# Performance work log

Measured on AMD Instinct MI355X. Metric: run time of the kernel, lower is better.

The kernel has to match this reference:

```python
import jax, jax.numpy as jnp
import numpy as np

B, S, H, OUT = 64, 513, 1024, 128   # batch, seq (incl CLS), hidden, slot labels
T = S - 1                            # subword tokens after dropping [CLS]
P_WORD_START = 0.75                  # avg ~1.33 subwords per word


def setup_inputs() -> dict:
    key = jax.random.key(0)
    k1, k2, k3, k4 = jax.random.split(key, 4)
    hidden_states = jax.random.normal(k1, (B, S, H), jnp.float32)
    W = jax.random.normal(k2, (H, OUT), jnp.float32) * 0.02
    b = jax.random.normal(k3, (OUT,), jnp.float32) * 0.02
    # contiguous, non-decreasing word ids: cumsum of word-start flags
    starts = (jax.random.uniform(k4, (B, T)) < P_WORD_START).astype(jnp.int32)
    starts = starts.at[:, 0].set(1)
    segment_ids = jnp.cumsum(starts, axis=-1) - 1  # [B, T], values in [0, n_words)
    return {"hidden_states": hidden_states, "W": W, "b": b,
            "segment_ids": segment_ids}


def _merge_row(logits, seg):
    # logits: [T, OUT], seg: [T] contiguous non-decreasing word ids
    s = jax.ops.segment_sum(logits, seg, num_segments=T)                    # [T, OUT]
    c = jax.ops.segment_sum(jnp.ones((T,), logits.dtype), seg, num_segments=T)
    mean = s / jnp.maximum(c, 1.0)[:, None]
    # words beyond n_words (empty segments) -> zero padding, as in the original
    return jnp.where(c[:, None] > 0, mean, 0.0)


def reference(hidden_states, W, b, segment_ids):
    x = hidden_states[:, 1:]                       # drop [CLS]; dropout = identity (eval)
    logits = jnp.einsum('bth,ho->bto', x, W) + b   # [B, T, OUT]
    merged = jax.vmap(_merge_row)(logits, segment_ids)  # per-word ragged mean + pad
    return jnp.transpose(merged, (0, 2, 1))        # [B, OUT, T]
```

## Files before the change

kernel.cpp:

```cpp
#include <hip/hip_runtime.h>
#include <hip/hip_bf16.h>

#define B_    64
#define S_    513
#define T_    512
#define H_    1024
#define OUT_  128
#define BK    32
#define BN    32
#define NKT   (H_ / BK)

typedef __attribute__((ext_vector_type(8))) short short8_t;
typedef __attribute__((ext_vector_type(4))) float f32x4;

__device__ inline ushort f2bf(float f) {
    union { float f; unsigned u; } x; x.f = f;
    unsigned r = x.u + 0x7fffu + ((x.u >> 16) & 1u);
    return (ushort)(r >> 16);
}

union SmemT {
    struct {
        ushort As[2][T_ * BK];
        ushort Bs[2][BN * BK];
    } st;
    float lg[T_ * 33];
};

__global__ __launch_bounds__(512, 2) void fused_kernel(
    const float* __restrict__ hs, const float* __restrict__ W,
    const float* __restrict__ bias, const int* __restrict__ seg,
    float* __restrict__ out)
{
    __shared__ SmemT sm;
    __shared__ int s_start[T_];
    __shared__ int s_cnt[T_];

    int d = blockIdx.x;
    int batch = (d & 7) + ((d >> 5) << 3);
    int o0    = ((d >> 3) & 3) * BN;

    int tid  = threadIdx.x;
    int lane = tid & 63;
    int w    = tid >> 6;
    int l15  = lane & 15, ksl = lane >> 4;

    s_start[tid] = T_;
    s_cnt[tid]   = 0;
    __syncthreads();
    {
        int sid = seg[batch * T_ + tid];
        atomicMin(&s_start[sid], tid);
        atomicAdd(&s_cnt[sid], 1);
    }

    int arow = tid >> 3;
    int ac8  = tid & 7;
    const float* aptr = hs + ((size_t)(batch * S_ + 1 + arow)) * H_ + ac8 * 4;
    int wAbase = arow * BK + ((((ac8 >> 1) ^ ((arow >> 1) & 3))) << 3)
               + ((ac8 & 1) << 2);

    int wk = tid >> 4;
    int wo = (tid & 15) * 2;
    const float* wptr = W + (size_t)wk * OUT_ + o0 + wo;
    int wBo0 = wo * BK + (((wk >> 3) ^ ((wo >> 1) & 3)) << 3) + (wk & 7);

    int rAo[4], rBo[2];
#pragma unroll
    for (int fm = 0; fm < 4; ++fm) {
        int row = w * 64 + fm * 16 + l15;
        rAo[fm] = row * BK + ((ksl ^ ((row >> 1) & 3)) << 3);
    }
#pragma unroll
    for (int fn = 0; fn < 2; ++fn) {
        int o = fn * 16 + l15;
        rBo[fn] = o * BK + ((ksl ^ ((o >> 1) & 3)) << 3);
    }

    f32x4 acc[4][2];
#pragma unroll
    for (int fm = 0; fm < 4; ++fm)
#pragma unroll
        for (int fn = 0; fn < 2; ++fn) acc[fm][fn] = (f32x4){0.f, 0.f, 0.f, 0.f};

    float4 ra[8];
    float2 rw;

    auto loadT = [&](int kt) {
        const float* ap = aptr + kt * BK;
#pragma unroll
        for (int p = 0; p < 8; ++p)
            ra[p] = *reinterpret_cast<const float4*>(ap + (size_t)p * 64 * H_);
        rw = *reinterpret_cast<const float2*>(wptr + (size_t)kt * BK * OUT_);
    };
    auto writeT = [&](int nb) {
#pragma unroll
        for (int p = 0; p < 8; ++p) {
            union { ushort u[4]; uint2 v; } pk;
            pk.u[0] = f2bf(ra[p].x); pk.u[1] = f2bf(ra[p].y);
            pk.u[2] = f2bf(ra[p].z); pk.u[3] = f2bf(ra[p].w);
            *reinterpret_cast<uint2*>(&sm.st.As[nb][wAbase + p * 64 * BK]) = pk.v;
        }
        sm.st.Bs[nb][wBo0]      = f2bf(rw.x);
        sm.st.Bs[nb][wBo0 + BK] = f2bf(rw.y);
    };
    auto computeT = [&](int cb) {
        short8_t af[4], bfr[2];
#pragma unroll
        for (int fm = 0; fm < 4; ++fm)
            af[fm] = *reinterpret_cast<const short8_t*>(&sm.st.As[cb][rAo[fm]]);
#pragma unroll
        for (int fn = 0; fn < 2; ++fn)
            bfr[fn] = *reinterpret_cast<const short8_t*>(&sm.st.Bs[cb][rBo[fn]]);
#pragma unroll
        for (int fm = 0; fm < 4; ++fm)
#pragma unroll
            for (int fn = 0; fn < 2; ++fn)
                acc[fm][fn] = __builtin_amdgcn_mfma_f32_16x16x32_bf16(
                    af[fm], bfr[fn], acc[fm][fn], 0, 0, 0);
    };

    loadT(0);
    writeT(0);
    __syncthreads();

    for (int kt = 0; kt < NKT; ++kt) {
        int cb = kt & 1;
        if (kt + 1 < NKT) loadT(kt + 1);
        computeT(cb);
        if (kt + 1 < NKT) writeT(cb ^ 1);
        __syncthreads();
    }

    float bv0 = bias[o0 + l15];
    float bv1 = bias[o0 + 16 + l15];
#pragma unroll
    for (int fm = 0; fm < 4; ++fm) {
#pragma unroll
        for (int fn = 0; fn < 2; ++fn) {
            float bv = fn ? bv1 : bv0;
            int o = fn * 16 + l15;
#pragma unroll
            for (int r = 0; r < 4; ++r) {
                int t = w * 64 + fm * 16 + ksl * 4 + r;
                sm.lg[t * 33 + o] = acc[fm][fn][r] + bv;
            }
        }
    }
    __syncthreads();

#pragma unroll
    for (int it = 0; it < 32; ++it) {
        int idx = tid + it * 512;
        int o   = idx >> 9;
        int s   = idx & 511;
        int cnt = s_cnt[s];
        float v = 0.f;
        if (cnt > 0) {
            int st = s_start[s];
            float sum = 0.f;
            for (int i = 0; i < cnt; ++i)
                sum += sm.lg[(st + i) * 33 + o];
            v = sum / (float)cnt;
        }
        out[((size_t)batch * OUT_ + o0 + o) * T_ + s] = v;
    }
}

extern "C" void kernel_launch(void* const* d_in, const int* in_sizes, int n_in,
                              void* d_out, int out_size, void* d_ws, size_t ws_size,
                              hipStream_t stream) {
    const float* hs   = (const float*)d_in[0];
    const float* W    = (const float*)d_in[1];
    const float* bias = (const float*)d_in[2];
    const int*   seg  = (const int*)d_in[3];
    float* out = (float*)d_out;

    fused_kernel<<<B_ * (OUT_ / BN), 512, 0, stream>>>(hs, W, bias, seg, out);
}
```

Baseline: 59.42 us.

## Tile over tokens instead of outputs, pretranspose W to bf16, and handle halo segments

The fused kernel used to have each block handle a full 512-token row for 32 output columns, so every hidden-state row was read four times. Now each block owns 64 tokens across all 128 outputs and loads up to 96 rows so that words crossing the tile edge can be finished locally. A separate small kernel first converts W to bf16 and transposes it into the workspace, so B fragments can be loaded straight into registers without going through LDS. The costs are an extra kernel launch, halo rows that are loaded and multiplied redundantly, and more involved boundary logic for segments that span tiles. Bias is now added after the mean, and tile 7 zero-fills the output for empty trailing words.

```diff
diff --git a/kernel.cpp b/kernel.cpp
--- a/kernel.cpp
+++ b/kernel.cpp
@@ -7,8 +7,10 @@
 #define H_    1024
 #define OUT_  128
 #define BK    32
-#define BN    32
 #define NKT   (H_ / BK)
+#define ROWS  96
+#define OWN   64
+#define LGS   132
 
 typedef __attribute__((ext_vector_type(8))) short short8_t;
 typedef __attribute__((ext_vector_type(4))) float f32x4;
@@ -18,152 +20,188 @@
     unsigned r = x.u + 0x7fffu + ((x.u >> 16) & 1u);
     return (ushort)(r >> 16);
 }
-
-union SmemT {
-    struct {
-        ushort As[2][T_ * BK];
-        ushort Bs[2][BN * BK];
-    } st;
-    float lg[T_ * 33];
-};
-
-__global__ __launch_bounds__(512, 2) void fused_kernel(
-    const float* __restrict__ hs, const float* __restrict__ W,
+__device__ inline int4 pack8(const float4& a, const float4& b) {
+    union { ushort u[8]; int4 v; } pk;
+    pk.u[0] = f2bf(a.x); pk.u[1] = f2bf(a.y); pk.u[2] = f2bf(a.z); pk.u[3] = f2bf(a.w);
+    pk.u[4] = f2bf(b.x); pk.u[5] = f2bf(b.y); pk.u[6] = f2bf(b.z); pk.u[7] = f2bf(b.w);
+    return pk.v;
+}
+
+__global__ __launch_bounds__(256) void wt_kernel(
+    const float* __restrict__ W, ushort* __restrict__ Wt)
+{
+    __shared__ ushort tile[64][65];
+    int k0 = blockIdx.x * 64, o0 = blockIdx.y * 64;
+    int tid = threadIdx.x;
+#pragma unroll
+    for (int p = 0; p < 16; ++p) {
+        int idx = tid + p * 256;
+        int r = idx >> 6, c = idx & 63;
+        tile[r][c] = f2bf(W[(size_t)(k0 + r) * OUT_ + o0 + c]);
+    }
+    __syncthreads();
+#pragma unroll
+    for (int p = 0; p < 16; ++p) {
+        int idx = tid + p * 256;
+        int c = idx >> 6, r = idx & 63;
+        Wt[(size_t)(o0 + c) * H_ + k0 + r] = tile[r][c];
+    }
+}
+
+__global__ __launch_bounds__(256, 2) void fused_kernel(
+    const float* __restrict__ hs, const ushort* __restrict__ Wt,
     const float* __restrict__ bias, const int* __restrict__ seg,
     float* __restrict__ out)
 {
-    __shared__ SmemT sm;
-    __shared__ int s_start[T_];
-    __shared__ int s_cnt[T_];
-
-    int d = blockIdx.x;
-    int batch = (d & 7) + ((d >> 5) << 3);
-    int o0    = ((d >> 3) & 3) * BN;
+    union Smem {
+        ushort As[2][ROWS * BK];
+        float  lg[ROWS * LGS];
+    };
+    __shared__ Smem sm;
+    __shared__ int sseg[ROWS];
+    __shared__ int lstart[OWN];
+    __shared__ int lcnt[OWN];
+    __shared__ int sExt, sSlo;
+
+    int bid  = blockIdx.x;
+    int b    = bid >> 3;
+    int tile = bid & 7;
+    int t0   = tile * OWN;
+    int Tl   = (T_ - t0) < ROWS ? (T_ - t0) : ROWS;
 
     int tid  = threadIdx.x;
     int lane = tid & 63;
     int w    = tid >> 6;
+    int wm   = w & 1, wn = w >> 1;
     int l15  = lane & 15, ksl = lane >> 4;
 
-    s_start[tid] = T_;
-    s_cnt[tid]   = 0;
-    __syncthreads();
-    {
-        int sid = seg[batch * T_ + tid];
-        atomicMin(&s_start[sid], tid);
-        atomicAdd(&s_cnt[sid], 1);
-    }
-
-    int arow = tid >> 3;
-    int ac8  = tid & 7;
-    const float* aptr = hs + ((size_t)(batch * S_ + 1 + arow)) * H_ + ac8 * 4;
-    int wAbase = arow * BK + ((((ac8 >> 1) ^ ((arow >> 1) & 3))) << 3)
-               + ((ac8 & 1) << 2);
-
-    int wk = tid >> 4;
-    int wo = (tid & 15) * 2;
-    const float* wptr = W + (size_t)wk * OUT_ + o0 + wo;
-    int wBo0 = wo * BK + (((wk >> 3) ^ ((wo >> 1) & 3)) << 3) + (wk & 7);
-
-    int rAo[4], rBo[2];
-#pragma unroll
-    for (int fm = 0; fm < 4; ++fm) {
-        int row = w * 64 + fm * 16 + l15;
-        rAo[fm] = row * BK + ((ksl ^ ((row >> 1) & 3)) << 3);
-    }
-#pragma unroll
-    for (int fn = 0; fn < 2; ++fn) {
-        int o = fn * 16 + l15;
-        rBo[fn] = o * BK + ((ksl ^ ((o >> 1) & 3)) << 3);
-    }
-
-    f32x4 acc[4][2];
-#pragma unroll
-    for (int fm = 0; fm < 4; ++fm)
-#pragma unroll
-        for (int fn = 0; fn < 2; ++fn) acc[fm][fn] = (f32x4){0.f, 0.f, 0.f, 0.f};
-
-    float4 ra[8];
-    float2 rw;
-
-    auto loadT = [&](int kt) {
-        const float* ap = aptr + kt * BK;
-#pragma unroll
-        for (int p = 0; p < 8; ++p)
-            ra[p] = *reinterpret_cast<const float4*>(ap + (size_t)p * 64 * H_);
-        rw = *reinterpret_cast<const float2*>(wptr + (size_t)kt * BK * OUT_);
-    };
-    auto writeT = [&](int nb) {
-#pragma unroll
-        for (int p = 0; p < 8; ++p) {
-            union { ushort u[4]; uint2 v; } pk;
-            pk.u[0] = f2bf(ra[p].x); pk.u[1] = f2bf(ra[p].y);
-            pk.u[2] = f2bf(ra[p].z); pk.u[3] = f2bf(ra[p].w);
-            *reinterpret_cast<uint2*>(&sm.st.As[nb][wAbase + p * 64 * BK]) = pk.v;
+    if (tid < Tl)  sseg[tid] = seg[b * T_ + t0 + tid];
+    if (tid < OWN) { lstart[tid] = ROWS; lcnt[tid] = 0; }
+    if (tid == 0)  sExt = Tl;
+    __syncthreads();
+    if (tid == 0) {
+        int start0 = (t0 == 0) || (seg[b * T_ + t0 - 1] != sseg[0]);
+        sSlo = sseg[0] + (start0 ? 0 : 1);
+    }
+    if (tid >= OWN && tid < Tl && sseg[tid] != sseg[tid - 1])
+        atomicMin(&sExt, tid);
+    __syncthreads();
+    int ext  = sExt;
+    int s_lo = sSlo;
+    int s_hi = sseg[OWN - 1] + 1;
+    if (tid < ext && sseg[tid] >= s_lo) {
+        int li = sseg[tid] - s_lo;
+        atomicMin(&lstart[li], tid);
+        atomicAdd(&lcnt[li], 1);
+    }
+
+    int arow0 = tid >> 2;
+    int ac    = tid & 3;
+    int arow1 = 64 + arow0;
+    const float* aptr0 = hs + ((size_t)(b * S_ + 1 + t0 + arow0)) * H_ + ac * 8;
+    const float* aptr1 = hs + ((size_t)(b * S_ + 1 + t0 + arow1)) * H_ + ac * 8;
+    bool doC1 = (tid < 128) && (arow1 < ext);
+    int wA0 = arow0 * BK + ac * 8;
+    int wA1 = arow1 * BK + ac * 8;
+
+    const ushort* bp[4];
+#pragma unroll
+    for (int fn = 0; fn < 4; ++fn)
+        bp[fn] = Wt + (size_t)(wn * 64 + fn * 16 + l15) * H_ + ksl * 8;
+
+    f32x4 acc[3][4];
+#pragma unroll
+    for (int fm = 0; fm < 3; ++fm)
+#pragma unroll
+        for (int fn = 0; fn < 4; ++fn) acc[fm][fn] = (f32x4){0.f, 0.f, 0.f, 0.f};
+
+    float4 ra0, ra1, ra2, ra3;
+    short8_t bfA[4], bfB[4];
+
+    auto loadA = [&](int kt) {
+        const float* p = aptr0 + kt * BK;
+        ra0 = *reinterpret_cast<const float4*>(p);
+        ra1 = *reinterpret_cast<const float4*>(p + 4);
+        if (doC1) {
+            const float* q = aptr1 + kt * BK;
+            ra2 = *reinterpret_cast<const float4*>(q);
+            ra3 = *reinterpret_cast<const float4*>(q + 4);
         }
-        sm.st.Bs[nb][wBo0]      = f2bf(rw.x);
-        sm.st.Bs[nb][wBo0 + BK] = f2bf(rw.y);
-    };
-    auto computeT = [&](int cb) {
-        short8_t af[4], bfr[2];
-#pragma unroll
-        for (int fm = 0; fm < 4; ++fm)
-            af[fm] = *reinterpret_cast<const short8_t*>(&sm.st.As[cb][rAo[fm]]);
-#pragma unroll
-        for (int fn = 0; fn < 2; ++fn)
-            bfr[fn] = *reinterpret_cast<const short8_t*>(&sm.st.Bs[cb][rBo[fn]]);
-#pragma unroll
-        for (int fm = 0; fm < 4; ++fm)
-#pragma unroll
-            for (int fn = 0; fn < 2; ++fn)
+    };
+    auto loadB = [&](short8_t* dst, int kt) {
+#pragma unroll
+        for (int fn = 0; fn < 4; ++fn)
+            dst[fn] = *reinterpret_cast<const short8_t*>(bp[fn] + kt * BK);
+    };
+    auto writeA = [&](int nb) {
+        *reinterpret_cast<int4*>(&sm.As[nb][wA0]) = pack8(ra0, ra1);
+        if (doC1)
+            *reinterpret_cast<int4*>(&sm.As[nb][wA1]) = pack8(ra2, ra3);
+    };
+    auto compute = [&](int cb, short8_t* bf) {
+        short8_t af[3];
+#pragma unroll
+        for (int fm = 0; fm < 3; ++fm)
+            af[fm] = *reinterpret_cast<const short8_t*>(
+                &sm.As[cb][(wm * 48 + fm * 16 + l15) * BK + ksl * 8]);
+#pragma unroll
+        for (int fm = 0; fm < 3; ++fm)
+#pragma unroll
+            for (int fn = 0; fn < 4; ++fn)
                 acc[fm][fn] = __builtin_amdgcn_mfma_f32_16x16x32_bf16(
-                    af[fm], bfr[fn], acc[fm][fn], 0, 0, 0);
-    };
-
-    loadT(0);
-    writeT(0);
-    __syncthreads();
-
-    for (int kt = 0; kt < NKT; ++kt) {
-        int cb = kt & 1;
-        if (kt + 1 < NKT) loadT(kt + 1);
-        computeT(cb);
-        if (kt + 1 < NKT) writeT(cb ^ 1);
+                    af[fm], bf[fn], acc[fm][fn], 0, 0, 0);
+    };
+
+    loadB(bfA, 0); loadA(0);
+    writeA(0);
+    __syncthreads();
+
+    for (int kt = 0; kt < NKT; kt += 2) {
+        loadA(kt + 1); loadB(bfB, kt + 1);
+        compute(0, bfA);
+        writeA(1);
         __syncthreads();
-    }
-
-    float bv0 = bias[o0 + l15];
-    float bv1 = bias[o0 + 16 + l15];
-#pragma unroll
-    for (int fm = 0; fm < 4; ++fm) {
-#pragma unroll
-        for (int fn = 0; fn < 2; ++fn) {
-            float bv = fn ? bv1 : bv0;
-            int o = fn * 16 + l15;
-#pragma unroll
-            for (int r = 0; r < 4; ++r) {
-                int t = w * 64 + fm * 16 + ksl * 4 + r;
-                sm.lg[t * 33 + o] = acc[fm][fn][r] + bv;
-            }
+        bool more = (kt + 2 < NKT);
+        if (more) { loadA(kt + 2); loadB(bfA, kt + 2); }
+        compute(1, bfB);
+        if (more) writeA(0);
+        __syncthreads();
+    }
+
+#pragma unroll
+    for (int fm = 0; fm < 3; ++fm) {
+        int rbase = wm * 48 + fm * 16 + ksl * 4;
+#pragma unroll
+        for (int fn = 0; fn < 4; ++fn) {
+            int o = wn * 64 + fn * 16 + l15;
+#pragma unroll
+            for (int r = 0; r < 4; ++r)
+                sm.lg[(rbase + r) * LGS + o] = acc[fm][fn][r];
         }
     }
     __syncthreads();
 
-#pragma unroll
-    for (int it = 0; it < 32; ++it) {
-        int idx = tid + it * 512;
-        int o   = idx >> 9;
-        int s   = idx & 511;
-        int cnt = s_cnt[s];
-        float v = 0.f;
-        if (cnt > 0) {
-            int st = s_start[s];
+    int sl   = tid & 63;
+    int ogrp = tid >> 6;
+    int ns   = s_hi - s_lo;
+    if (sl < ns) {
+        int st = lstart[sl];
+        int cn = lcnt[sl];
+        float inv = 1.0f / (float)cn;
+        float* dst = out + (size_t)b * OUT_ * T_ + s_lo + sl;
+#pragma unroll 4
+        for (int oi = 0; oi < 32; ++oi) {
+            int o = ogrp + oi * 4;
             float sum = 0.f;
-            for (int i = 0; i < cnt; ++i)
-                sum += sm.lg[(st + i) * 33 + o];
-            v = sum / (float)cnt;
+            for (int i = 0; i < cn; ++i) sum += sm.lg[(st + i) * LGS + o];
+            dst[(size_t)o * T_] = sum * inv + bias[o];
         }
-        out[((size_t)batch * OUT_ + o0 + o) * T_ + s] = v;
+    }
+
+    if (tile == 7) {
+        for (int o = ogrp; o < OUT_; o += 4)
+            for (int s = s_hi + sl; s < T_; s += 64)
+                out[((size_t)b * OUT_ + o) * T_ + s] = 0.f;
     }
 }
 
@@ -176,5 +214,8 @@
     const int*   seg  = (const int*)d_in[3];
     float* out = (float*)d_out;
 
-    fused_kernel<<<B_ * (OUT_ / BN), 512, 0, stream>>>(hs, W, bias, seg, out);
-}
+    ushort* Wt = (ushort*)d_ws;
+
+    wt_kernel<<<dim3(H_ / 64, OUT_ / 64), 256, 0, stream>>>(W, Wt);
+    fused_kernel<<<B_ * (T_ / OWN), 256, 0, stream>>>(hs, Wt, bias, seg, out);
+}
```

After: 64.86 us. 1.09x slower.
